# Performance work log

Hardware: AMD Instinct MI355X
Metric: run time of the kernel (lower is better)

Reference implementation:

```python
import jax, jax.numpy as jnp
import numpy as np

T, B, D_IN, H, ALPHA = 512, 32, 41, 800, 20
BOND_LENS = np.array([1.458, 1.525, 1.330], dtype=np.float32)   # N-CA, CA-C, C-N (Angstrom)
BOND_ANGS = np.array([2.124, 1.941, 2.028], dtype=np.float32)   # supplementary bond angles (rad)


def _lstm_dir(x, Wih, Whh, b, reverse):
    # x: [T,B,in] -> hidden states [T,B,H] for one direction
    xs = jnp.einsum('tbi,gi->tbg', x, Wih) + b  # precompute input projections [T,B,4H]
    if reverse:
        xs = xs[::-1]
    h0 = jnp.zeros((x.shape[1], Whh.shape[1]), x.dtype)

    def step(carry, xg):
        h, c = carry
        g = xg + h @ Whh.T
        i, f, gg, o = jnp.split(g, 4, axis=-1)
        c = jax.nn.sigmoid(f) * c + jax.nn.sigmoid(i) * jnp.tanh(gg)
        h = jax.nn.sigmoid(o) * jnp.tanh(c)
        return (h, c), h

    _, hs = jax.lax.scan(step, (h0, h0), xs)
    return hs[::-1] if reverse else hs


def _bilstm(x, Wf, Uf, bf, Wb, Ub, bb):
    return jnp.concatenate([_lstm_dir(x, Wf, Uf, bf, False),
                            _lstm_dir(x, Wb, Ub, bb, True)], axis=-1)


def _calculate_dihedrals(p, alphabet):
    # p: [T,B,ALPHA] softmax weights; alphabet: [ALPHA,3] learned angles
    y = p @ jnp.sin(alphabet)
    xc = p @ jnp.cos(alphabet)
    return jnp.arctan2(y, xc)  # [T,B,3]


def _calculate_coordinates(angles):
    # NeRF-style recursive extension: 3 backbone atoms per residue.
    t, b, _ = angles.shape
    tors = angles.transpose(0, 2, 1).reshape(3 * t, b)          # [3T,B]
    r = jnp.tile(jnp.asarray(BOND_LENS), t)                      # [3T]
    th = jnp.tile(jnp.asarray(BOND_ANGS), t)                     # [3T]
    a0 = jnp.broadcast_to(jnp.array([0.0, 0.0, 0.0], angles.dtype), (b, 3))
    b0 = jnp.broadcast_to(jnp.array([1.458, 0.0, 0.0], angles.dtype), (b, 3))
    c0 = jnp.broadcast_to(jnp.array([2.0, 1.0, 0.0], angles.dtype), (b, 3))

    def _norm(v):
        return v / jnp.linalg.norm(v, axis=-1, keepdims=True)

    def step(carry, inp):
        pa, pb, pc = carry
        phi, rr, tt = inp                                        # phi:[B], rr/tt scalar
        bc = _norm(pc - pb)
        n = _norm(jnp.cross(pb - pa, bc))
        m = jnp.cross(n, bc)
        d = (pc - rr * jnp.cos(tt) * bc
             + (rr * jnp.sin(tt)) * (jnp.cos(phi)[:, None] * m + jnp.sin(phi)[:, None] * n))
        return (pb, pc, d), d

    _, coords = jax.lax.scan(step, (a0, b0, c0), (tors, r, th))
    return coords  # [3T,B,3]


def setup_inputs() -> dict:
    key = jax.random.key(0)
    ks = jax.random.split(key, 16)
    s = 0.05
    d = {"x": jax.random.normal(ks[0], (T, B, D_IN), jnp.float32)}
    ins = [D_IN, 2 * H]
    i = 1
    for l in range(2):
        for dname in ("f", "b"):
            d[f"Wih_{dname}{l}"] = jax.random.normal(ks[i], (4 * H, ins[l]), jnp.float32) * s; i += 1
            d[f"Whh_{dname}{l}"] = jax.random.normal(ks[i], (4 * H, H), jnp.float32) * s; i += 1
            d[f"b_{dname}{l}"] = jnp.zeros((4 * H,), jnp.float32)
    d["Wl"] = jax.random.normal(ks[13], (ALPHA, 2 * H), jnp.float32) * s
    d["bl"] = jnp.zeros((ALPHA,), jnp.float32)
    d["alphabet"] = jax.random.uniform(ks[14], (ALPHA, 3), jnp.float32, -np.pi, np.pi)
    return d


def reference(x, Wih_f0, Whh_f0, b_f0, Wih_b0, Whh_b0, b_b0,
              Wih_f1, Whh_f1, b_f1, Wih_b1, Whh_b1, b_b1,
              Wl, bl, alphabet):
    h1 = _bilstm(x, Wih_f0, Whh_f0, b_f0, Wih_b0, Whh_b0, b_b0)   # [T,B,2H]
    h2 = _bilstm(h1, Wih_f1, Whh_f1, b_f1, Wih_b1, Whh_b1, b_b1)  # [T,B,2H]
    logits = jnp.einsum('tbh,ah->tba', h2, Wl) + bl
    p = jax.nn.softmax(logits, axis=-1)
    angles = _calculate_dihedrals(p, alphabet)                     # [T,B,3]
    return _calculate_coordinates(angles)                          # [3T,B,3]
```

## Files before the change

### kernel.cpp

```cpp
#include <hip/hip_runtime.h>
#include <math.h>


#define TT 512
#define BB 32
#define HH 800
#define DIN 41
#define KROW 1600

typedef _Float16 f16;
typedef _Float16 half8 __attribute__((ext_vector_type(8)));
typedef float floatx4 __attribute__((ext_vector_type(4)));
typedef unsigned uint4v __attribute__((ext_vector_type(4)));

#define OFF_XT   8192
#define OFF_H1   (OFF_XT + 524288)
#define OFF_H2   (OFF_H1 + 13107200)
#define OFF_ANG  (OFF_H2 + 13107200)
#define OFF_SIN  (OFF_ANG + 49152)
#define OFF_COS  (OFF_SIN + 64)

#define SENT 0xFFFFFFFFFFFFFFFFull

__device__ __forceinline__ float sigm(float x) { return 1.0f / (1.0f + expf(-x)); }

union U64H8 { unsigned long long u[2]; half8 h; };

__device__ __forceinline__ unsigned long long ald8(const f16* p) {
    return __hip_atomic_load((const unsigned long long*)p, __ATOMIC_RELAXED, __HIP_MEMORY_SCOPE_AGENT);
}
__device__ __forceinline__ void ast8(f16* p, unsigned long long v) {
    __hip_atomic_store((unsigned long long*)p, v, __ATOMIC_RELAXED, __HIP_MEMORY_SCOPE_AGENT);
}
__device__ __forceinline__ half8 cvt8(const float* p) {
    half8 r;
#pragma unroll
    for (int i = 0; i < 8; ++i) r[i] = (f16)p[i];
    return r;
}

__device__ __forceinline__ size_t hpi(int t, int KT, int q, int b) {
    return ((((size_t)t * 50 + KT) * 4 + q) * 32 + b) * 8;
}

__global__ __launch_bounds__(512, 1) void rnn0_kernel(
    const f16* __restrict__ xp, f16* __restrict__ h1,
    const float* __restrict__ Wih_f0, const float* __restrict__ Whh_f0, const float* __restrict__ b_f0,
    const float* __restrict__ Wih_b0, const float* __restrict__ Whh_b0, const float* __restrict__ b_b0)
{
    __shared__ float gbuf[8][32][33];
    __shared__ f16  hbuf[256];

    const int tid  = threadIdx.x;
    const int w    = tid >> 6;
    const int lane = tid & 63;
    const int l15  = lane & 15;
    const int quad = lane >> 4;
    const int dir  = blockIdx.x / 100;
    const int blk  = blockIdx.x % 100;
    const int j0   = blk * 8;
    const int jl   = tid >> 5;
    const int bb   = tid & 31;

    const float* Wih = dir ? Wih_b0 : Wih_f0;
    const float* Whh = dir ? Whh_b0 : Whh_f0;
    const float* bs  = dir ? b_b0  : b_f0;

    half8 afr[2][4];
#pragma unroll
    for (int mt = 0; mt < 2; ++mt) {
        const int r = mt * 16 + l15;
        const int grow = (r >> 3) * HH + j0 + (r & 7);
#pragma unroll
        for (int i = 0; i < 4; ++i) {
            const int kt = w + 8 * i;
            half8 v;
#pragma unroll
            for (int jj = 0; jj < 8; ++jj) v[jj] = (f16)0.f;
            if (kt < 27) {
                if (kt < 2) {
#pragma unroll
                    for (int jj = 0; jj < 8; ++jj) {
                        const int k = kt * 32 + quad * 8 + jj;
                        if (k < DIN) v[jj] = (f16)Wih[(size_t)grow * DIN + k];
                    }
                } else {
                    v = cvt8(Whh + (size_t)grow * HH + (kt - 2) * 32 + quad * 8);
                }
            }
            afr[mt][i] = v;
        }
    }
    const float bi = bs[0 * HH + j0 + jl], bf = bs[1 * HH + j0 + jl],
                bg = bs[2 * HH + j0 + jl], bo = bs[3 * HH + j0 + jl];

    const int KT0 = dir * 25 + (blk >> 2);
    const int q0  = blk & 3;

    float creg = 0.0f;
    for (int s = 0; s < TT; ++s) {
        const int t  = dir ? (TT - 1 - s) : s;
        const int tp = dir ? t + 1 : t - 1;

        U64H8 rb[4][2];
        if (s > 0) {
#pragma unroll
            for (int i = 0; i < 4; ++i) {
                const int kt = w + 8 * i;
                if (kt >= 2 && kt < 27) {
                    const f16* p = h1 + hpi(tp, dir * 25 + (kt - 2), quad, 0);
                    rb[i][0].u[0] = ald8(p + (size_t)l15 * 8);
                    rb[i][0].u[1] = ald8(p + (size_t)l15 * 8 + 4);
                    rb[i][1].u[0] = ald8(p + (size_t)(16 + l15) * 8);
                    rb[i][1].u[1] = ald8(p + (size_t)(16 + l15) * 8 + 4);
                }
            }
        }

        floatx4 acc[2][2];
        acc[0][0] = (floatx4)0.f; acc[0][1] = (floatx4)0.f;
        acc[1][0] = (floatx4)0.f; acc[1][1] = (floatx4)0.f;

        if (w < 2) {
            const f16* p = xp + ((((size_t)t * 2 + w) * 4 + quad) * 32) * 8;
            const half8 b0 = *(const half8*)(p + (size_t)l15 * 8);
            const half8 b1 = *(const half8*)(p + (size_t)(16 + l15) * 8);
            acc[0][0] = __builtin_amdgcn_mfma_f32_16x16x32_f16(afr[0][0], b0, acc[0][0], 0, 0, 0);
            acc[0][1] = __builtin_amdgcn_mfma_f32_16x16x32_f16(afr[0][0], b1, acc[0][1], 0, 0, 0);
            acc[1][0] = __builtin_amdgcn_mfma_f32_16x16x32_f16(afr[1][0], b0, acc[1][0], 0, 0, 0);
            acc[1][1] = __builtin_amdgcn_mfma_f32_16x16x32_f16(afr[1][0], b1, acc[1][1], 0, 0, 0);
        }

        if (s > 0) {
#pragma unroll
            for (int i = 0; i < 4; ++i) {
                const int kt = w + 8 * i;
                if (kt >= 2 && kt < 27) {
                    const f16* p = h1 + hpi(tp, dir * 25 + (kt - 2), quad, 0);
                    for (;;) {
                        const int bad = (rb[i][0].u[0] == SENT) | (rb[i][0].u[1] == SENT) |
                                        (rb[i][1].u[0] == SENT) | (rb[i][1].u[1] == SENT);
                        if (!__any(bad)) break;
                        __builtin_amdgcn_s_sleep(1);
                        rb[i][0].u[0] = ald8(p + (size_t)l15 * 8);
                        rb[i][0].u[1] = ald8(p + (size_t)l15 * 8 + 4);
                        rb[i][1].u[0] = ald8(p + (size_t)(16 + l15) * 8);
                        rb[i][1].u[1] = ald8(p + (size_t)(16 + l15) * 8 + 4);
                    }
                    acc[0][0] = __builtin_amdgcn_mfma_f32_16x16x32_f16(afr[0][i], rb[i][0].h, acc[0][0], 0, 0, 0);
                    acc[0][1] = __builtin_amdgcn_mfma_f32_16x16x32_f16(afr[0][i], rb[i][1].h, acc[0][1], 0, 0, 0);
                    acc[1][0] = __builtin_amdgcn_mfma_f32_16x16x32_f16(afr[1][i], rb[i][0].h, acc[1][0], 0, 0, 0);
                    acc[1][1] = __builtin_amdgcn_mfma_f32_16x16x32_f16(afr[1][i], rb[i][1].h, acc[1][1], 0, 0, 0);
                }
            }
        }

#pragma unroll
        for (int mt = 0; mt < 2; ++mt)
#pragma unroll
            for (int nt = 0; nt < 2; ++nt)
#pragma unroll
                for (int rg = 0; rg < 4; ++rg)
                    gbuf[w][mt * 16 + quad * 4 + rg][nt * 16 + l15] = acc[mt][nt][rg];
        __syncthreads();
        if (tid < 256) {
            float gi_ = bi, gf_ = bf, gc_ = bg, go_ = bo;
#pragma unroll
            for (int ww = 0; ww < 8; ++ww) {
                gi_ += gbuf[ww][jl][bb];
                gf_ += gbuf[ww][8 + jl][bb];
                gc_ += gbuf[ww][16 + jl][bb];
                go_ += gbuf[ww][24 + jl][bb];
            }
            const float cn = sigm(gf_) * creg + sigm(gi_) * tanhf(gc_);
            creg = cn;
            hbuf[bb * 8 + jl] = (f16)(sigm(go_) * tanhf(cn));
        }
        __syncthreads();
        if (tid < BB) {
            f16* dst = h1 + hpi(t, KT0, q0, tid);
            const unsigned long long* src = (const unsigned long long*)(hbuf + tid * 8);
            ast8(dst, src[0]);
            ast8(dst + 4, src[1]);
        }
    }
}

__global__ __launch_bounds__(512, 1) void rnn1_kernel(
    const f16* __restrict__ h1, f16* __restrict__ h2,
    const float* __restrict__ Wih_f1, const float* __restrict__ Whh_f1, const float* __restrict__ b_f1,
    const float* __restrict__ Wih_b1, const float* __restrict__ Whh_b1, const float* __restrict__ b_b1)
{
    __shared__ float gbuf[8][32][33];
    __shared__ f16  hbuf[256];

    const int tid  = threadIdx.x;
    const int w    = tid >> 6;
    const int lane = tid & 63;
    const int l15  = lane & 15;
    const int quad = lane >> 4;
    const int dir  = blockIdx.x / 100;
    const int blk  = blockIdx.x % 100;
    const int j0   = blk * 8;
    const int jl   = tid >> 5;
    const int bb   = tid & 31;

    const float* Wih = dir ? Wih_b1 : Wih_f1;
    const float* Whh = dir ? Whh_b1 : Whh_f1;
    const float* bs  = dir ? b_b1  : b_f1;

    half8 afr[2][10];
#pragma unroll
    for (int mt = 0; mt < 2; ++mt) {
        const int r = mt * 16 + l15;
        const int grow = (r >> 3) * HH + j0 + (r & 7);
#pragma unroll
        for (int i = 0; i < 10; ++i) {
            const int kt = w + 8 * i;
            half8 v;
#pragma unroll
            for (int jj = 0; jj < 8; ++jj) v[jj] = (f16)0.f;
            if (kt < 75) {
                if (kt < 50) v = cvt8(Wih + (size_t)grow * KROW + kt * 32 + quad * 8);
                else         v = cvt8(Whh + (size_t)grow * HH + (kt - 50) * 32 + quad * 8);
            }
            afr[mt][i] = v;
        }
    }
    const float bi = bs[0 * HH + j0 + jl], bf = bs[1 * HH + j0 + jl],
                bg = bs[2 * HH + j0 + jl], bo = bs[3 * HH + j0 + jl];

    const int KT0 = dir * 25 + (blk >> 2);
    const int q0  = blk & 3;

    float creg = 0.0f;
    for (int s = 0; s < TT; ++s) {
        const int t  = dir ? (TT - 1 - s) : s;
        const int tp = dir ? t + 1 : t - 1;

        U64H8 rb[10][2];
        if (s > 0) {
#pragma unroll
            for (int i = 0; i < 10; ++i) {
                const int kt = w + 8 * i;
                if (kt >= 50 && kt < 75) {
                    const f16* p = h2 + hpi(tp, dir * 25 + (kt - 50), quad, 0);
                    rb[i][0].u[0] = ald8(p + (size_t)l15 * 8);
                    rb[i][0].u[1] = ald8(p + (size_t)l15 * 8 + 4);
                    rb[i][1].u[0] = ald8(p + (size_t)(16 + l15) * 8);
                    rb[i][1].u[1] = ald8(p + (size_t)(16 + l15) * 8 + 4);
                }
            }
        }

        floatx4 acc[2][2];
        acc[0][0] = (floatx4)0.f; acc[0][1] = (floatx4)0.f;
        acc[1][0] = (floatx4)0.f; acc[1][1] = (floatx4)0.f;

#pragma unroll
        for (int i = 0; i < 7; ++i) {
            const int kt = w + 8 * i;
            if (kt < 50) {
                const f16* p = h1 + hpi(t, kt, quad, 0);
                const half8 b0 = *(const half8*)(p + (size_t)l15 * 8);
                const half8 b1 = *(const half8*)(p + (size_t)(16 + l15) * 8);
                acc[0][0] = __builtin_amdgcn_mfma_f32_16x16x32_f16(afr[0][i], b0, acc[0][0], 0, 0, 0);
                acc[0][1] = __builtin_amdgcn_mfma_f32_16x16x32_f16(afr[0][i], b1, acc[0][1], 0, 0, 0);
                acc[1][0] = __builtin_amdgcn_mfma_f32_16x16x32_f16(afr[1][i], b0, acc[1][0], 0, 0, 0);
                acc[1][1] = __builtin_amdgcn_mfma_f32_16x16x32_f16(afr[1][i], b1, acc[1][1], 0, 0, 0);
            }
        }

        if (s > 0) {
#pragma unroll
            for (int i = 0; i < 10; ++i) {
                const int kt = w + 8 * i;
                if (kt >= 50 && kt < 75) {
                    const f16* p = h2 + hpi(tp, dir * 25 + (kt - 50), quad, 0);
                    for (;;) {
                        const int bad = (rb[i][0].u[0] == SENT) | (rb[i][0].u[1] == SENT) |
                                        (rb[i][1].u[0] == SENT) | (rb[i][1].u[1] == SENT);
                        if (!__any(bad)) break;
                        __builtin_amdgcn_s_sleep(1);
                        rb[i][0].u[0] = ald8(p + (size_t)l15 * 8);
                        rb[i][0].u[1] = ald8(p + (size_t)l15 * 8 + 4);
                        rb[i][1].u[0] = ald8(p + (size_t)(16 + l15) * 8);
                        rb[i][1].u[1] = ald8(p + (size_t)(16 + l15) * 8 + 4);
                    }
                    acc[0][0] = __builtin_amdgcn_mfma_f32_16x16x32_f16(afr[0][i], rb[i][0].h, acc[0][0], 0, 0, 0);
                    acc[0][1] = __builtin_amdgcn_mfma_f32_16x16x32_f16(afr[0][i], rb[i][1].h, acc[0][1], 0, 0, 0);
                    acc[1][0] = __builtin_amdgcn_mfma_f32_16x16x32_f16(afr[1][i], rb[i][0].h, acc[1][0], 0, 0, 0);
                    acc[1][1] = __builtin_amdgcn_mfma_f32_16x16x32_f16(afr[1][i], rb[i][1].h, acc[1][1], 0, 0, 0);
                }
            }
        }

#pragma unroll
        for (int mt = 0; mt < 2; ++mt)
#pragma unroll
            for (int nt = 0; nt < 2; ++nt)
#pragma unroll
                for (int rg = 0; rg < 4; ++rg)
                    gbuf[w][mt * 16 + quad * 4 + rg][nt * 16 + l15] = acc[mt][nt][rg];
        __syncthreads();
        if (tid < 256) {
            float gi_ = bi, gf_ = bf, gc_ = bg, go_ = bo;
#pragma unroll
            for (int ww = 0; ww < 8; ++ww) {
                gi_ += gbuf[ww][jl][bb];
                gf_ += gbuf[ww][8 + jl][bb];
                gc_ += gbuf[ww][16 + jl][bb];
                go_ += gbuf[ww][24 + jl][bb];
            }
            const float cn = sigm(gf_) * creg + sigm(gi_) * tanhf(gc_);
            creg = cn;
            hbuf[bb * 8 + jl] = (f16)(sigm(go_) * tanhf(cn));
        }
        __syncthreads();
        if (tid < BB) {
            f16* dst = h2 + hpi(t, KT0, q0, tid);
            const unsigned long long* src = (const unsigned long long*)(hbuf + tid * 8);
            ast8(dst, src[0]);
            ast8(dst + 4, src[1]);
        }
    }
}

__global__ void prep_kernel(const float* __restrict__ x, const float* __restrict__ alphabet,
                            f16* __restrict__ xp, float* __restrict__ sin_t,
                            float* __restrict__ cos_t, unsigned* __restrict__ hsent) {
    const int gid = blockIdx.x * blockDim.x + threadIdx.x;
    const int nth = gridDim.x * blockDim.x;
    for (int idx = gid; idx < TT * BB * 64; idx += nth) {
        const int tb = idx >> 6;
        const int i  = idx & 63;
        const int t  = tb >> 5;
        const int b  = tb & 31;
        const size_t di = ((((size_t)t * 2 + (i >> 5)) * 4 + ((i >> 3) & 3)) * 32 + b) * 8 + (i & 7);
        xp[di] = (i < DIN) ? (f16)x[(size_t)tb * DIN + i] : (f16)0.f;
    }
    uint4v* hs4 = (uint4v*)hsent;
    const uint4v sv = {0xFFFFFFFFu, 0xFFFFFFFFu, 0xFFFFFFFFu, 0xFFFFFFFFu};
    const int n4 = (2 * 13107200) / 4;
    for (int idx = gid; idx < n4; idx += nth) hs4[idx] = sv;
    if (gid < 60) { sin_t[gid] = sinf(alphabet[gid]); cos_t[gid] = cosf(alphabet[gid]); }
}

__global__ __launch_bounds__(640, 1) void head_kernel(
    const f16* __restrict__ h2, const float* __restrict__ Wl, const float* __restrict__ bl,
    const float* __restrict__ sin_t, const float* __restrict__ cos_t,
    float* __restrict__ angles) {
    __shared__ float pl[20][33];
    __shared__ float mx[32];
    const int t = blockIdx.x;
    const int a = threadIdx.x / 32;
    const int b = threadIdx.x & 31;
    if (a < 20) {
        float acc = bl[a];
        const float* wr = Wl + (size_t)a * KROW;
        const f16*   hr = h2 + (size_t)t * 50 * 4 * 32 * 8;
        for (int k8 = 0; k8 < KROW / 8; ++k8) {
            const half8 hv = *(const half8*)(hr + (((size_t)k8) * 32 + b) * 8);
#pragma unroll
            for (int j = 0; j < 8; ++j) acc = fmaf(wr[k8 * 8 + j], (float)hv[j], acc);
        }
        pl[a][b] = acc;
    }
    __syncthreads();
    if (threadIdx.x < 32) {
        float m = pl[0][threadIdx.x];
        for (int i = 1; i < 20; ++i) m = fmaxf(m, pl[i][threadIdx.x]);
        mx[threadIdx.x] = m;
    }
    __syncthreads();
    if (a < 20) pl[a][b] = expf(pl[a][b] - mx[b]);
    __syncthreads();
    if (threadIdx.x < 96) {
        const int c = threadIdx.x / 32, b2 = threadIdx.x & 31;
        float y = 0.f, xx = 0.f;
        for (int i = 0; i < 20; ++i) {
            const float e = pl[i][b2];
            y  = fmaf(e, sin_t[i * 3 + c], y);
            xx = fmaf(e, cos_t[i * 3 + c], xx);
        }
        angles[((size_t)t * BB + b2) * 3 + c] = atan2f(y, xx);
    }
}

__global__ void coords_kernel(const float* __restrict__ angles, float* __restrict__ out) {
    const int b = threadIdx.x;
    if (b >= BB) return;
    const float rs[3]  = {1.458f, 1.525f, 1.33f};
    const float ths[3] = {2.124f, 1.941f, 2.028f};
    float ct[3], st[3];
#pragma unroll
    for (int k = 0; k < 3; ++k) { ct[k] = cosf(ths[k]); st[k] = sinf(ths[k]); }
    float pax = 0.f,     pay = 0.f, paz = 0.f;
    float pbx = 1.458f,  pby = 0.f, pbz = 0.f;
    float pcx = 2.f,     pcy = 1.f, pcz = 0.f;
    for (int n = 0; n < 3 * TT; ++n) {
        const int t = n / 3;
        const int k = n - 3 * t;
        const float phi = angles[((size_t)t * BB + b) * 3 + k];
        float ux = pcx - pbx, uy = pcy - pby, uz = pcz - pbz;
        const float il = rsqrtf(ux * ux + uy * uy + uz * uz);
        const float bcx = ux * il, bcy = uy * il, bcz = uz * il;
        const float wx = pbx - pax, wy = pby - pay, wz = pbz - paz;
        float cx = wy * bcz - wz * bcy, cy = wz * bcx - wx * bcz, cz = wx * bcy - wy * bcx;
        const float iln = rsqrtf(cx * cx + cy * cy + cz * cz);
        const float nx = cx * iln, ny = cy * iln, nz = cz * iln;
        const float mxv = ny * bcz - nz * bcy, myv = nz * bcx - nx * bcz, mzv = nx * bcy - ny * bcx;
        float sp, cp;
        __sincosf(phi, &sp, &cp);
        const float rr = rs[k], cth = ct[k], sth = st[k];
        const float dx = pcx - rr * cth * bcx + rr * sth * (cp * mxv + sp * nx);
        const float dy = pcy - rr * cth * bcy + rr * sth * (cp * myv + sp * ny);
        const float dz = pcz - rr * cth * bcz + rr * sth * (cp * mzv + sp * nz);
        float* o = out + ((size_t)n * BB + b) * 3;
        o[0] = dx; o[1] = dy; o[2] = dz;
        pax = pbx; pay = pby; paz = pbz;
        pbx = pcx; pby = pcy; pbz = pcz;
        pcx = dx;  pcy = dy;  pcz = dz;
    }
}

extern "C" void kernel_launch(void* const* d_in, const int* in_sizes, int n_in,
                              void* d_out, int out_size, void* d_ws, size_t ws_size,
                              hipStream_t stream) {
    (void)in_sizes; (void)n_in; (void)out_size; (void)ws_size;
    const float* x      = (const float*)d_in[0];
    const float* Wih_f0 = (const float*)d_in[1];
    const float* Whh_f0 = (const float*)d_in[2];
    const float* b_f0   = (const float*)d_in[3];
    const float* Wih_b0 = (const float*)d_in[4];
    const float* Whh_b0 = (const float*)d_in[5];
    const float* b_b0   = (const float*)d_in[6];
    const float* Wih_f1 = (const float*)d_in[7];
    const float* Whh_f1 = (const float*)d_in[8];
    const float* b_f1   = (const float*)d_in[9];
    const float* Wih_b1 = (const float*)d_in[10];
    const float* Whh_b1 = (const float*)d_in[11];
    const float* b_b1   = (const float*)d_in[12];
    const float* Wl     = (const float*)d_in[13];
    const float* bl     = (const float*)d_in[14];
    const float* alphabet = (const float*)d_in[15];

    float* ws = (float*)d_ws;
    f16*   xp     = (f16*)(ws + OFF_XT);
    f16*   h1     = (f16*)(ws + OFF_H1);
    f16*   h2     = (f16*)(ws + OFF_H2);
    float* angles = ws + OFF_ANG;
    float* sin_t  = ws + OFF_SIN;
    float* cos_t  = ws + OFF_COS;

    prep_kernel<<<1024, 256, 0, stream>>>(x, alphabet, xp, sin_t, cos_t, (unsigned*)(ws + OFF_H1));
    rnn0_kernel<<<200, 512, 0, stream>>>(xp, h1,
        Wih_f0, Whh_f0, b_f0, Wih_b0, Whh_b0, b_b0);
    rnn1_kernel<<<200, 512, 0, stream>>>(h1, h2,
        Wih_f1, Whh_f1, b_f1, Wih_b1, Whh_b1, b_b1);
    head_kernel<<<TT, 640, 0, stream>>>(h2, Wl, bl, sin_t, cos_t, angles);
    coords_kernel<<<1, 64, 0, stream>>>(angles, (float*)d_out);
}
```

Before: 4.948 ms.

## Prefetch next-step input fragments and batch sentinel polling in LSTM recurrence

Both recurrent kernels now load the non-recurrent operand (x projection in layer 0, h1 in layer 1) for step t+1 into registers during step t, which moves that global load latency off the per-step critical path. The sentinel spin-wait now reissues loads for all not-yet-ready tiles together and drops the sleep, so the wave waits one round-trip per retry instead of one per tile. The gbuf row pitch changes from 33 to 34 floats, which alters the LDS bank mapping of the accumulator scatter and gather. The cost is more live registers for the prefetch buffers and tighter polling that puts more load traffic on memory.

```diff
diff --git a/kernel.cpp b/kernel.cpp
--- a/kernel.cpp
+++ b/kernel.cpp
@@ -48,7 +48,7 @@
     const float* __restrict__ Wih_f0, const float* __restrict__ Whh_f0, const float* __restrict__ b_f0,
     const float* __restrict__ Wih_b0, const float* __restrict__ Whh_b0, const float* __restrict__ b_b0)
 {
-    __shared__ float gbuf[8][32][33];
+    __shared__ float gbuf[8][32][34];
     __shared__ f16  hbuf[256];
 
     const int tid  = threadIdx.x;
@@ -97,10 +97,21 @@
     const int KT0 = dir * 25 + (blk >> 2);
     const int q0  = blk & 3;
 
+    half8 px0, px1;
+    {
+        const int t0 = dir ? (TT - 1) : 0;
+        if (w < 2) {
+            const f16* p = xp + ((((size_t)t0 * 2 + w) * 4 + quad) * 32) * 8;
+            px0 = *(const half8*)(p + (size_t)l15 * 8);
+            px1 = *(const half8*)(p + (size_t)(16 + l15) * 8);
+        }
+    }
+
     float creg = 0.0f;
     for (int s = 0; s < TT; ++s) {
         const int t  = dir ? (TT - 1 - s) : s;
         const int tp = dir ? t + 1 : t - 1;
+        const int tn = dir ? (t > 0 ? t - 1 : 0) : (t < TT - 1 ? t + 1 : t);
 
         U64H8 rb[4][2];
         if (s > 0) {
@@ -122,31 +133,58 @@
         acc[1][0] = (floatx4)0.f; acc[1][1] = (floatx4)0.f;
 
         if (w < 2) {
-            const f16* p = xp + ((((size_t)t * 2 + w) * 4 + quad) * 32) * 8;
-            const half8 b0 = *(const half8*)(p + (size_t)l15 * 8);
-            const half8 b1 = *(const half8*)(p + (size_t)(16 + l15) * 8);
-            acc[0][0] = __builtin_amdgcn_mfma_f32_16x16x32_f16(afr[0][0], b0, acc[0][0], 0, 0, 0);
-            acc[0][1] = __builtin_amdgcn_mfma_f32_16x16x32_f16(afr[0][0], b1, acc[0][1], 0, 0, 0);
-            acc[1][0] = __builtin_amdgcn_mfma_f32_16x16x32_f16(afr[1][0], b0, acc[1][0], 0, 0, 0);
-            acc[1][1] = __builtin_amdgcn_mfma_f32_16x16x32_f16(afr[1][0], b1, acc[1][1], 0, 0, 0);
+            acc[0][0] = __builtin_amdgcn_mfma_f32_16x16x32_f16(afr[0][0], px0, acc[0][0], 0, 0, 0);
+            acc[0][1] = __builtin_amdgcn_mfma_f32_16x16x32_f16(afr[0][0], px1, acc[0][1], 0, 0, 0);
+            acc[1][0] = __builtin_amdgcn_mfma_f32_16x16x32_f16(afr[1][0], px0, acc[1][0], 0, 0, 0);
+            acc[1][1] = __builtin_amdgcn_mfma_f32_16x16x32_f16(afr[1][0], px1, acc[1][1], 0, 0, 0);
+            const f16* p = xp + ((((size_t)tn * 2 + w) * 4 + quad) * 32) * 8;
+            px0 = *(const half8*)(p + (size_t)l15 * 8);
+            px1 = *(const half8*)(p + (size_t)(16 + l15) * 8);
         }
 
         if (s > 0) {
+            int dm = 0;
 #pragma unroll
             for (int i = 0; i < 4; ++i) {
                 const int kt = w + 8 * i;
                 if (kt >= 2 && kt < 27) {
-                    const f16* p = h1 + hpi(tp, dir * 25 + (kt - 2), quad, 0);
-                    for (;;) {
-                        const int bad = (rb[i][0].u[0] == SENT) | (rb[i][0].u[1] == SENT) |
-                                        (rb[i][1].u[0] == SENT) | (rb[i][1].u[1] == SENT);
-                        if (!__any(bad)) break;
-                        __builtin_amdgcn_s_sleep(1);
-                        rb[i][0].u[0] = ald8(p + (size_t)l15 * 8);
-                        rb[i][0].u[1] = ald8(p + (size_t)l15 * 8 + 4);
-                        rb[i][1].u[0] = ald8(p + (size_t)(16 + l15) * 8);
-                        rb[i][1].u[1] = ald8(p + (size_t)(16 + l15) * 8 + 4);
+                    const int bad = (rb[i][0].u[0] == SENT) | (rb[i][0].u[1] == SENT) |
+                                    (rb[i][1].u[0] == SENT) | (rb[i][1].u[1] == SENT);
+                    dm |= bad << i;
+                }
+            }
+            while (__any(dm != 0)) {
+#pragma unroll
+                for (int i = 0; i < 4; ++i) {
+                    const int kt = w + 8 * i;
+                    if (kt >= 2 && kt < 27) {
+                        if (dm & (1 << i)) {
+                            const f16* p = h1 + hpi(tp, dir * 25 + (kt - 2), quad, 0);
+                            rb[i][0].u[0] = ald8(p + (size_t)l15 * 8);
+                            rb[i][0].u[1] = ald8(p + (size_t)l15 * 8 + 4);
+                            rb[i][1].u[0] = ald8(p + (size_t)(16 + l15) * 8);
+                            rb[i][1].u[1] = ald8(p + (size_t)(16 + l15) * 8 + 4);
+                        }
                     }
+                }
+                int nm = 0;
+#pragma unroll
+                for (int i = 0; i < 4; ++i) {
+                    const int kt = w + 8 * i;
+                    if (kt >= 2 && kt < 27) {
+                        if (dm & (1 << i)) {
+                            const int bad = (rb[i][0].u[0] == SENT) | (rb[i][0].u[1] == SENT) |
+                                            (rb[i][1].u[0] == SENT) | (rb[i][1].u[1] == SENT);
+                            nm |= bad << i;
+                        }
+                    }
+                }
+                dm = nm;
+            }
+#pragma unroll
+            for (int i = 0; i < 4; ++i) {
+                const int kt = w + 8 * i;
+                if (kt >= 2 && kt < 27) {
                     acc[0][0] = __builtin_amdgcn_mfma_f32_16x16x32_f16(afr[0][i], rb[i][0].h, acc[0][0], 0, 0, 0);
                     acc[0][1] = __builtin_amdgcn_mfma_f32_16x16x32_f16(afr[0][i], rb[i][1].h, acc[0][1], 0, 0, 0);
                     acc[1][0] = __builtin_amdgcn_mfma_f32_16x16x32_f16(afr[1][i], rb[i][0].h, acc[1][0], 0, 0, 0);
@@ -191,7 +229,7 @@
     const float* __restrict__ Wih_f1, const float* __restrict__ Whh_f1, const float* __restrict__ b_f1,
     const float* __restrict__ Wih_b1, const float* __restrict__ Whh_b1, const float* __restrict__ b_b1)
 {
-    __shared__ float gbuf[8][32][33];
+    __shared__ float gbuf[8][32][34];
     __shared__ f16  hbuf[256];
 
     const int tid  = threadIdx.x;
@@ -233,22 +271,37 @@
     const int KT0 = dir * 25 + (blk >> 2);
     const int q0  = blk & 3;
 
+    half8 pa[7][2];
+    {
+        const int t0 = dir ? (TT - 1) : 0;
+#pragma unroll
+        for (int i = 0; i < 7; ++i) {
+            const int kt = w + 8 * i;
+            if (kt < 50) {
+                const f16* p = h1 + hpi(t0, kt, quad, 0);
+                pa[i][0] = *(const half8*)(p + (size_t)l15 * 8);
+                pa[i][1] = *(const half8*)(p + (size_t)(16 + l15) * 8);
+            }
+        }
+    }
+
     float creg = 0.0f;
     for (int s = 0; s < TT; ++s) {
         const int t  = dir ? (TT - 1 - s) : s;
         const int tp = dir ? t + 1 : t - 1;
-
-        U64H8 rb[10][2];
+        const int tn = dir ? (t > 0 ? t - 1 : 0) : (t < TT - 1 ? t + 1 : t);
+
+        U64H8 rb[4][2];
         if (s > 0) {
 #pragma unroll
-            for (int i = 0; i < 10; ++i) {
+            for (int i = 6; i < 10; ++i) {
                 const int kt = w + 8 * i;
                 if (kt >= 50 && kt < 75) {
                     const f16* p = h2 + hpi(tp, dir * 25 + (kt - 50), quad, 0);
-                    rb[i][0].u[0] = ald8(p + (size_t)l15 * 8);
-                    rb[i][0].u[1] = ald8(p + (size_t)l15 * 8 + 4);
-                    rb[i][1].u[0] = ald8(p + (size_t)(16 + l15) * 8);
-                    rb[i][1].u[1] = ald8(p + (size_t)(16 + l15) * 8 + 4);
+                    rb[i - 6][0].u[0] = ald8(p + (size_t)l15 * 8);
+                    rb[i - 6][0].u[1] = ald8(p + (size_t)l15 * 8 + 4);
+                    rb[i - 6][1].u[0] = ald8(p + (size_t)(16 + l15) * 8);
+                    rb[i - 6][1].u[1] = ald8(p + (size_t)(16 + l15) * 8 + 4);
                 }
             }
         }
@@ -261,36 +314,70 @@
         for (int i = 0; i < 7; ++i) {
             const int kt = w + 8 * i;
             if (kt < 50) {
-                const f16* p = h1 + hpi(t, kt, quad, 0);
-                const half8 b0 = *(const half8*)(p + (size_t)l15 * 8);
-                const half8 b1 = *(const half8*)(p + (size_t)(16 + l15) * 8);
-                acc[0][0] = __builtin_amdgcn_mfma_f32_16x16x32_f16(afr[0][i], b0, acc[0][0], 0, 0, 0);
-                acc[0][1] = __builtin_amdgcn_mfma_f32_16x16x32_f16(afr[0][i], b1, acc[0][1], 0, 0, 0);
-                acc[1][0] = __builtin_amdgcn_mfma_f32_16x16x32_f16(afr[1][i], b0, acc[1][0], 0, 0, 0);
-                acc[1][1] = __builtin_amdgcn_mfma_f32_16x16x32_f16(afr[1][i], b1, acc[1][1], 0, 0, 0);
+                acc[0][0] = __builtin_amdgcn_mfma_f32_16x16x32_f16(afr[0][i], pa[i][0], acc[0][0], 0, 0, 0);
+                acc[0][1] = __builtin_amdgcn_mfma_f32_16x16x32_f16(afr[0][i], pa[i][1], acc[0][1], 0, 0, 0);
+                acc[1][0] = __builtin_amdgcn_mfma_f32_16x16x32_f16(afr[1][i], pa[i][0], acc[1][0], 0, 0, 0);
+                acc[1][1] = __builtin_amdgcn_mfma_f32_16x16x32_f16(afr[1][i], pa[i][1], acc[1][1], 0, 0, 0);
+            }
+        }
+
+#pragma unroll
+        for (int i = 0; i < 7; ++i) {
+            const int kt = w + 8 * i;
+            if (kt < 50) {
+                const f16* p = h1 + hpi(tn, kt, quad, 0);
+                pa[i][0] = *(const half8*)(p + (size_t)l15 * 8);
+                pa[i][1] = *(const half8*)(p + (size_t)(16 + l15) * 8);
             }
         }
 
         if (s > 0) {
-#pragma unroll
-            for (int i = 0; i < 10; ++i) {
+            int dm = 0;
+#pragma unroll
+            for (int i = 6; i < 10; ++i) {
                 const int kt = w + 8 * i;
                 if (kt >= 50 && kt < 75) {
-                    const f16* p = h2 + hpi(tp, dir * 25 + (kt - 50), quad, 0);
-                    for (;;) {
-                        const int bad = (rb[i][0].u[0] == SENT) | (rb[i][0].u[1] == SENT) |
-                                        (rb[i][1].u[0] == SENT) | (rb[i][1].u[1] == SENT);
-                        if (!__any(bad)) break;
-                        __builtin_amdgcn_s_sleep(1);
-                        rb[i][0].u[0] = ald8(p + (size_t)l15 * 8);
-                        rb[i][0].u[1] = ald8(p + (size_t)l15 * 8 + 4);
-                        rb[i][1].u[0] = ald8(p + (size_t)(16 + l15) * 8);
-                        rb[i][1].u[1] = ald8(p + (size_t)(16 + l15) * 8 + 4);
+                    const int bad = (rb[i - 6][0].u[0] == SENT) | (rb[i - 6][0].u[1] == SENT) |
+                                    (rb[i - 6][1].u[0] == SENT) | (rb[i - 6][1].u[1] == SENT);
+                    dm |= bad << (i - 6);
+                }
+            }
+            while (__any(dm != 0)) {
+#pragma unroll
+                for (int i = 6; i < 10; ++i) {
+                    const int kt = w + 8 * i;
+                    if (kt >= 50 && kt < 75) {
+                        if (dm & (1 << (i - 6))) {
+                            const f16* p = h2 + hpi(tp, dir * 25 + (kt - 50), quad, 0);
+                            rb[i - 6][0].u[0] = ald8(p + (size_t)l15 * 8);
+                            rb[i - 6][0].u[1] = ald8(p + (size_t)l15 * 8 + 4);
+                            rb[i - 6][1].u[0] = ald8(p + (size_t)(16 + l15) * 8);
+                            rb[i - 6][1].u[1] = ald8(p + (size_t)(16 + l15) * 8 + 4);
+                        }
                     }
-                    acc[0][0] = __builtin_amdgcn_mfma_f32_16x16x32_f16(afr[0][i], rb[i][0].h, acc[0][0], 0, 0, 0);
-                    acc[0][1] = __builtin_amdgcn_mfma_f32_16x16x32_f16(afr[0][i], rb[i][1].h, acc[0][1], 0, 0, 0);
-                    acc[1][0] = __builtin_amdgcn_mfma_f32_16x16x32_f16(afr[1][i], rb[i][0].h, acc[1][0], 0, 0, 0);
-                    acc[1][1] = __builtin_amdgcn_mfma_f32_16x16x32_f16(afr[1][i], rb[i][1].h, acc[1][1], 0, 0, 0);
+                }
+                int nm = 0;
+#pragma unroll
+                for (int i = 6; i < 10; ++i) {
+                    const int kt = w + 8 * i;
+                    if (kt >= 50 && kt < 75) {
+                        if (dm & (1 << (i - 6))) {
+                            const int bad = (rb[i - 6][0].u[0] == SENT) | (rb[i - 6][0].u[1] == SENT) |
+                                            (rb[i - 6][1].u[0] == SENT) | (rb[i - 6][1].u[1] == SENT);
+                            nm |= bad << (i - 6);
+                        }
+                    }
+                }
+                dm = nm;
+            }
+#pragma unroll
+            for (int i = 6; i < 10; ++i) {
+                const int kt = w + 8 * i;
+                if (kt >= 50 && kt < 75) {
+                    acc[0][0] = __builtin_amdgcn_mfma_f32_16x16x32_f16(afr[0][i], rb[i - 6][0].h, acc[0][0], 0, 0, 0);
+                    acc[0][1] = __builtin_amdgcn_mfma_f32_16x16x32_f16(afr[0][i], rb[i - 6][1].h, acc[0][1], 0, 0, 0);
+                    acc[1][0] = __builtin_amdgcn_mfma_f32_16x16x32_f16(afr[1][i], rb[i - 6][0].h, acc[1][0], 0, 0, 0);
+                    acc[1][1] = __builtin_amdgcn_mfma_f32_16x16x32_f16(afr[1][i], rb[i - 6][1].h, acc[1][1], 0, 0, 0);
                 }
             }
         }
```

Result: faster. 4.455 ms (-10.0%).
